# Kernel optimization log

Hardware: AMD Instinct MI355X
Metric: run time of the kernel (lower is better)

## Reference

```python
import jax, jax.numpy as jnp
import numpy as np

D_MODEL = 1024
NHEAD = 16
DK = D_MODEL // NHEAD  # 64
B, S = 2, 2048


def setup_inputs() -> dict:
    key = jax.random.key(0)
    ks = jax.random.split(key, 8)
    Q = jax.random.normal(ks[0], (B, S, D_MODEL), dtype=jnp.float32)
    K = jax.random.normal(ks[1], (B, S, D_MODEL), dtype=jnp.float32)
    V = jax.random.normal(ks[2], (B, S, D_MODEL), dtype=jnp.float32)
    additive_mask = jax.random.normal(ks[3], (S, S), dtype=jnp.float32)
    key_padding_mask = jnp.zeros((B, S), dtype=jnp.int32)  # ignored by the module
    # Per-head projection weights, stacked over heads: [H, d_model, dk]
    scale = 1.0 / np.sqrt(D_MODEL)
    WQ = jax.random.normal(ks[4], (NHEAD, D_MODEL, DK), dtype=jnp.float32) * scale
    WK = jax.random.normal(ks[5], (NHEAD, D_MODEL, DK), dtype=jnp.float32) * scale
    WV = jax.random.normal(ks[6], (NHEAD, D_MODEL, DK), dtype=jnp.float32) * scale
    WO = jax.random.normal(ks[7], (D_MODEL, D_MODEL), dtype=jnp.float32) * scale
    return {"Q": Q, "K": K, "V": V, "additive_mask": additive_mask,
            "key_padding_mask": key_padding_mask,
            "WQ": WQ, "WK": WK, "WV": WV, "WO": WO}


def reference(Q, K, V, additive_mask, key_padding_mask, WQ, WK, WV, WO):
    # Per-head projections, batched over heads: [B, H, S, dk]
    q = jnp.einsum('bsd,hdk->bhsk', Q, WQ)
    k = jnp.einsum('bsd,hdk->bhsk', K, WK)
    v = jnp.einsum('bsd,hdk->bhsk', V, WV)
    # scores: [B, H, S, S]; mask broadcasts over batch and head
    scores = jnp.einsum('bhqk,bhsk->bhqs', q, k) / np.sqrt(DK)
    scores = scores + additive_mask[None, None, :, :]
    attn = jax.nn.softmax(scores, axis=-1)
    o = jnp.einsum('bhqs,bhsk->bhqk', attn, v)  # [B, H, S, dk]
    # concat heads in head order == transpose + reshape to [B, S, H*dk]
    o = o.transpose(0, 2, 1, 3).reshape(Q.shape[0], Q.shape[1], D_MODEL)
    return o @ WO
```

## Files before the change

kernel.cpp:

```cpp
#include <hip/hip_runtime.h>
#include <hip/hip_bf16.h>
#include <stdint.h>

#define D_MODEL 1024
#define NHEAD 16
#define DKH 64
#define BATCH 2
#define SEQ 2048
#define LOG2E 1.44269504088896f

typedef __bf16 bf16_t;
typedef __bf16 bf16x8 __attribute__((ext_vector_type(8)));
typedef float f32x4 __attribute__((ext_vector_type(4)));

__device__ __forceinline__ float fast_exp2(float x) {
#if __has_builtin(__builtin_amdgcn_exp2f)
  return __builtin_amdgcn_exp2f(x);
#else
  return exp2f(x);
#endif
}

__device__ __forceinline__ void gload_lds16(const bf16_t* g, bf16_t* l) {
  auto gp = (const __attribute__((address_space(1))) void*)(uintptr_t)g;
  auto lp = (__attribute__((address_space(3))) void*)(uintptr_t)l;
  __builtin_amdgcn_global_load_lds(gp, lp, 16, 0, 0);
}

__global__ void k_cvtw(const float* __restrict__ WQ, const float* __restrict__ WK,
                       const float* __restrict__ WV, const float* __restrict__ WO,
                       bf16_t* __restrict__ wt) {
  int j = blockIdx.x * 256 + threadIdx.x;
  int d = j & 1023, n = j >> 10;
  if (n < 3072) {
    int proj = n >> 10, h = (n >> 6) & 15, k = n & 63;
    const float* w = proj == 0 ? WQ : (proj == 1 ? WK : WV);
    float scale = proj == 0 ? (0.125f * LOG2E) : 1.0f;
    wt[j] = (bf16_t)(w[(h << 16) + (d << 6) + k] * scale);
  } else {
    wt[j] = (bf16_t)WO[(d << 10) + (n - 3072)];
  }
}

__global__ void k_maskg(const float* __restrict__ M, bf16_t* __restrict__ Mf) {
  int t = blockIdx.x * 256 + threadIdx.x;
  int c = t & 3, lane = (t >> 2) & 63;
  int kvt = (t >> 8) & 31, qt16 = t >> 13;
  int q = qt16 * 16 + (lane & 15);
  int kv = kvt * 64 + c * 16 + ((lane >> 4) << 2);
  float4 m4 = *reinterpret_cast<const float4*>(M + (size_t)q * SEQ + kv);
  bf16_t o[4];
  o[0] = (bf16_t)(m4.x * LOG2E); o[1] = (bf16_t)(m4.y * LOG2E);
  o[2] = (bf16_t)(m4.z * LOG2E); o[3] = (bf16_t)(m4.w * LOG2E);
  *reinterpret_cast<ushort4*>(Mf + (size_t)t * 4) = *reinterpret_cast<ushort4*>(o);
}

__device__ __forceinline__ int vperm(int u) {
  return ((u >> 5) << 5) | (((u >> 2) & 3) << 3) | (((u >> 4) & 1) << 2) | (u & 3);
}

__global__ __launch_bounds__(256)
void k_gemm_qkv(const float* __restrict__ Qs, const float* __restrict__ Ks32,
                const float* __restrict__ Vs32, const bf16_t* __restrict__ Bt,
                bf16_t* __restrict__ qh, bf16_t* __restrict__ Kf,
                bf16_t* __restrict__ Vf) {
  __shared__ __align__(16) bf16_t As[128 * 32];
  __shared__ __align__(16) bf16_t Bs[128 * 32];
  const int tid = threadIdx.x;
  const int lane = tid & 63, wave = tid >> 6;
  const int g = lane >> 4, lr = lane & 15;
  const int bid = blockIdx.x;
  const int xcd = bid & 7, jj = bid >> 3;
  const int bm = xcd * 4 + (jj & 3);
  const int bn = jj >> 2;
  const int pn = bn >> 3;
  const float* Ap32 = pn == 0 ? Qs : (pn == 1 ? Ks32 : Vs32);
  const int wm = (wave >> 1) << 6, wn = (wave & 1) << 6;
  const int arow = tid >> 1, ako = (tid & 1) << 4;
  const float* aptr = Ap32 + (size_t)(bm * 128 + arow) * 1024 + ako;
  f32x4 acc[4][4] = {};

  float4 fA0 = *reinterpret_cast<const float4*>(aptr);
  float4 fA1 = *reinterpret_cast<const float4*>(aptr + 4);
  float4 fA2 = *reinterpret_cast<const float4*>(aptr + 8);
  float4 fA3 = *reinterpret_cast<const float4*>(aptr + 12);

  for (int kt = 0; kt < 1024; kt += 32) {
#pragma unroll
    for (int cc = 0; cc < 2; cc++) {
      int c = tid + cc * 256;
      int row = c >> 2, ko = (c & 3) << 3;
      gload_lds16(Bt + (size_t)(bn * 128 + row) * 1024 + kt + ko, Bs + c * 8);
    }
    {
      bf16x8 o0, o1;
      o0[0] = (bf16_t)fA0.x; o0[1] = (bf16_t)fA0.y; o0[2] = (bf16_t)fA0.z; o0[3] = (bf16_t)fA0.w;
      o0[4] = (bf16_t)fA1.x; o0[5] = (bf16_t)fA1.y; o0[6] = (bf16_t)fA1.z; o0[7] = (bf16_t)fA1.w;
      o1[0] = (bf16_t)fA2.x; o1[1] = (bf16_t)fA2.y; o1[2] = (bf16_t)fA2.z; o1[3] = (bf16_t)fA2.w;
      o1[4] = (bf16_t)fA3.x; o1[5] = (bf16_t)fA3.y; o1[6] = (bf16_t)fA3.z; o1[7] = (bf16_t)fA3.w;
      *reinterpret_cast<bf16x8*>(As + arow * 32 + ako) = o0;
      *reinterpret_cast<bf16x8*>(As + arow * 32 + ako + 8) = o1;
    }
    if (kt + 32 < 1024) {
      const float* np = aptr + kt + 32;
      fA0 = *reinterpret_cast<const float4*>(np);
      fA1 = *reinterpret_cast<const float4*>(np + 4);
      fA2 = *reinterpret_cast<const float4*>(np + 8);
      fA3 = *reinterpret_cast<const float4*>(np + 12);
    }
    __syncthreads();
    bf16x8 af[4], bfr[4];
#pragma unroll
    for (int t = 0; t < 4; t++)
      af[t] = *reinterpret_cast<const bf16x8*>(As + (wm + t * 16 + lr) * 32 + g * 8);
#pragma unroll
    for (int t = 0; t < 4; t++)
      bfr[t] = *reinterpret_cast<const bf16x8*>(Bs + (wn + t * 16 + lr) * 32 + g * 8);
    __builtin_amdgcn_s_setprio(1);
#pragma unroll
    for (int i = 0; i < 4; i++)
#pragma unroll
      for (int j = 0; j < 4; j++)
        acc[i][j] = __builtin_amdgcn_mfma_f32_16x16x32_bf16(af[i], bfr[j], acc[i][j], 0, 0, 0);
    __builtin_amdgcn_s_setprio(0);
    __syncthreads();
  }

#pragma unroll
  for (int i = 0; i < 4; i++)
#pragma unroll
    for (int j = 0; j < 4; j++)
#pragma unroll
      for (int e = 0; e < 4; e++) {
        int row = (bm << 7) + wm + i * 16 + g * 4 + e;
        int col = ((bn & 7) << 7) + wn + j * 16 + lr;
        float v = acc[i][j][e];
        int b = row >> 11, s = row & 2047, h = col >> 6, d = col & 63;
        size_t tilebase = ((size_t)(((b << 4) + h) * 32) + (s >> 6)) * 4096;
        if (pn == 0) {
          qh[((size_t)(((b << 4) + h) * SEQ + s) << 6) + d] = (bf16_t)v;
        } else if (pn == 1) {
          int r = s & 63, u = (d >> 3) ^ (r & 7), e2 = d & 7;
          Kf[tilebase + r * 64 + u * 8 + e2] = (bf16_t)v;
        } else {
          int c6 = vperm(s & 63);
          int u = (c6 >> 3) ^ (d & 7), e2 = c6 & 7;
          Vf[tilebase + d * 64 + u * 8 + e2] = (bf16_t)v;
        }
      }
}

__global__ __launch_bounds__(256)
void k_gemm_wo(const bf16_t* __restrict__ A, const bf16_t* __restrict__ Bt,
               float* __restrict__ C) {
  __shared__ __align__(16) bf16_t As[64 * 32];
  __shared__ __align__(16) bf16_t Bs[128 * 32];
  const int tid = threadIdx.x;
  const int lane = tid & 63, wave = tid >> 6;
  const int g = lane >> 4, lr = lane & 15;
  const int bid = blockIdx.x;
  const int xcd = bid & 7, jj = bid >> 3;
  const int bm = xcd * 8 + (jj & 7);
  const int bn = jj >> 3;
  const int wm = (wave >> 1) << 5, wn = (wave & 1) << 6;
  f32x4 acc[2][4] = {};

  for (int kt = 0; kt < 1024; kt += 32) {
    {
      int row = tid >> 2, ko = (tid & 3) << 3;
      gload_lds16(A + (size_t)(bm * 64 + row) * 1024 + kt + ko, As + tid * 8);
    }
#pragma unroll
    for (int cc = 0; cc < 2; cc++) {
      int c = tid + cc * 256;
      int row = c >> 2, ko = (c & 3) << 3;
      gload_lds16(Bt + (size_t)(bn * 128 + row) * 1024 + kt + ko, Bs + c * 8);
    }
    __syncthreads();
    bf16x8 af[2], bfr[4];
#pragma unroll
    for (int t = 0; t < 2; t++)
      af[t] = *reinterpret_cast<const bf16x8*>(As + (wm + t * 16 + lr) * 32 + g * 8);
#pragma unroll
    for (int t = 0; t < 4; t++)
      bfr[t] = *reinterpret_cast<const bf16x8*>(Bs + (wn + t * 16 + lr) * 32 + g * 8);
    __builtin_amdgcn_s_setprio(1);
#pragma unroll
    for (int i = 0; i < 2; i++)
#pragma unroll
      for (int j = 0; j < 4; j++)
        acc[i][j] = __builtin_amdgcn_mfma_f32_16x16x32_bf16(af[i], bfr[j], acc[i][j], 0, 0, 0);
    __builtin_amdgcn_s_setprio(0);
    __syncthreads();
  }
#pragma unroll
  for (int i = 0; i < 2; i++)
#pragma unroll
    for (int j = 0; j < 4; j++)
#pragma unroll
      for (int e = 0; e < 4; e++) {
        int row = (bm << 6) + wm + i * 16 + g * 4 + e;
        int col = (bn << 7) + wn + j * 16 + lr;
        C[(size_t)row * D_MODEL + col] = acc[i][j][e];
      }
}

__global__ __launch_bounds__(512)
void k_attn4(const bf16_t* __restrict__ Qh, const bf16_t* __restrict__ Kf,
             const bf16_t* __restrict__ Vf, const bf16_t* __restrict__ Mf,
             bf16_t* __restrict__ O) {
  __shared__ __align__(16) bf16_t Ks[2][64 * 64];
  __shared__ __align__(16) bf16_t Vs[2][64 * 64];
  const int bid = blockIdx.x;
  const int xcd = bid & 7, loc = bid >> 3;
  const int bh = xcd * 4 + (loc >> 4);
  const int qtile = loc & 15;
  const int b = bh >> 4, h = bh & 15;
  const int tid = threadIdx.x, wave = tid >> 6, lane = tid & 63;
  const int g = lane >> 4, lr = lane & 15;
  const int qbase = qtile * 128 + wave * 16;
  const bf16_t* qp = Qh + (size_t)bh * SEQ * DKH;
  const bf16_t* kfp = Kf + (size_t)bh * 32 * 4096;
  const bf16_t* vfp = Vf + (size_t)bh * 32 * 4096;
  const int qt16 = qtile * 8 + wave;
  const bf16_t* mp = Mf + ((size_t)qt16 * 32 * 64 + lane) * 16;

  bf16x8 aq[2];
#pragma unroll
  for (int ks = 0; ks < 2; ks++)
    aq[ks] = *reinterpret_cast<const bf16x8*>(
        qp + (size_t)(qbase + lr) * DKH + ks * 32 + g * 8);

  f32x4 oacc[4] = {};
  f32x4 lacc = {};
  const bf16_t onev = (bf16_t)1.0f;
  const bf16x8 ones = {onev, onev, onev, onev, onev, onev, onev, onev};

  auto stage = [&](int buf, int kt) {
    gload_lds16(kfp + (size_t)kt * 4096 + tid * 8, &Ks[buf][tid * 8]);
    gload_lds16(vfp + (size_t)kt * 4096 + tid * 8, &Vs[buf][tid * 8]);
  };

  stage(0, 0);
  bf16x8 mva = *reinterpret_cast<const bf16x8*>(mp);
  bf16x8 mvb = *reinterpret_cast<const bf16x8*>(mp + 8);
  __syncthreads();

  for (int it = 0; it < SEQ / 64; ++it) {
    const int cur = it & 1;
    if (it + 1 < SEQ / 64) stage(cur ^ 1, it + 1);
    bf16x8 mna = mva, mnb = mvb;
    if (it + 1 < SEQ / 64) {
      const bf16_t* mn = mp + (size_t)(it + 1) * 1024;
      mna = *reinterpret_cast<const bf16x8*>(mn);
      mnb = *reinterpret_cast<const bf16x8*>(mn + 8);
    }

    const bf16_t* kb = Ks[cur];
    const bf16_t* vb = Vs[cur];

    f32x4 p[4];
#pragma unroll
    for (int c = 0; c < 4; c++) {
      int r = c * 16 + lr;
      bf16x8 bk0 = *reinterpret_cast<const bf16x8*>(kb + r * 64 + ((g ^ (lr & 7)) << 3));
      bf16x8 bk1 = *reinterpret_cast<const bf16x8*>(kb + r * 64 + (((4 + g) ^ (lr & 7)) << 3));
      __builtin_amdgcn_s_setprio(1);
      f32x4 a = {};
      a = __builtin_amdgcn_mfma_f32_16x16x32_bf16(bk0, aq[0], a, 0, 0, 0);
      a = __builtin_amdgcn_mfma_f32_16x16x32_bf16(bk1, aq[1], a, 0, 0, 0);
      __builtin_amdgcn_s_setprio(0);
      p[c] = a;
    }

    bf16x8 pa[2];
#pragma unroll
    for (int c = 0; c < 4; c++)
#pragma unroll
      for (int e = 0; e < 4; e++) {
        int idx = c * 4 + e;
        float mk = (float)(idx < 8 ? mva[idx] : mvb[idx - 8]);
        float x = p[c][e] + mk;
        float pe = fast_exp2(fminf(x, 60.f));
        pa[c >> 1][(c & 1) * 4 + e] = (bf16_t)pe;
      }

    lacc = __builtin_amdgcn_mfma_f32_16x16x32_bf16(pa[0], ones, lacc, 0, 0, 0);
    lacc = __builtin_amdgcn_mfma_f32_16x16x32_bf16(pa[1], ones, lacc, 0, 0, 0);

#pragma unroll
    for (int c2 = 0; c2 < 4; c2++) {
      int r = c2 * 16 + lr;
      bf16x8 bv0 = *reinterpret_cast<const bf16x8*>(vb + r * 64 + ((g ^ (lr & 7)) << 3));
      bf16x8 bv1 = *reinterpret_cast<const bf16x8*>(vb + r * 64 + (((4 + g) ^ (lr & 7)) << 3));
      __builtin_amdgcn_s_setprio(1);
      oacc[c2] = __builtin_amdgcn_mfma_f32_16x16x32_bf16(pa[0], bv0, oacc[c2], 0, 0, 0);
      oacc[c2] = __builtin_amdgcn_mfma_f32_16x16x32_bf16(pa[1], bv1, oacc[c2], 0, 0, 0);
      __builtin_amdgcn_s_setprio(0);
    }
    __syncthreads();
    mva = mna; mvb = mnb;
  }

  float inv[4];
#pragma unroll
  for (int e = 0; e < 4; e++) inv[e] = 1.0f / lacc[e];
#pragma unroll
  for (int c2 = 0; c2 < 4; c2++)
#pragma unroll
    for (int e = 0; e < 4; e++) {
      float v = oacc[c2][e] * inv[e];
      int row = qbase + g * 4 + e;
      int col = (h << 6) + c2 * 16 + lr;
      O[(size_t)(b * SEQ + row) * D_MODEL + col] = (bf16_t)v;
    }
}

extern "C" void kernel_launch(void* const* d_in, const int* in_sizes, int n_in,
                              void* d_out, int out_size, void* d_ws, size_t ws_size,
                              hipStream_t stream) {
  const float* Q  = (const float*)d_in[0];
  const float* K  = (const float*)d_in[1];
  const float* V  = (const float*)d_in[2];
  const float* M  = (const float*)d_in[3];
  const float* WQ = (const float*)d_in[5];
  const float* WK = (const float*)d_in[6];
  const float* WV = (const float*)d_in[7];
  const float* WO = (const float*)d_in[8];

  char* ws = (char*)d_ws;
  const size_t MB = 1 << 20;
  bf16_t* Mf    = (bf16_t*)(ws + 24 * MB);
  bf16_t* WqkvT = (bf16_t*)(ws + 32 * MB);
  bf16_t* WoT   = (bf16_t*)(ws + 38 * MB);
  bf16_t* qh    = (bf16_t*)(ws + 40 * MB);
  bf16_t* Kf    = (bf16_t*)(ws + 48 * MB);
  bf16_t* Vf    = (bf16_t*)(ws + 56 * MB);
  bf16_t* Ob    = (bf16_t*)(ws + 64 * MB);

  k_maskg<<<4096, 256, 0, stream>>>(M, Mf);
  k_cvtw<<<16384, 256, 0, stream>>>(WQ, WK, WV, WO, WqkvT);

  k_gemm_qkv<<<768, 256, 0, stream>>>(Q, K, V, WqkvT, qh, Kf, Vf);

  k_attn4<<<512, 512, 0, stream>>>(qh, Kf, Vf, Mf, Ob);

  k_gemm_wo<<<512, 256, 0, stream>>>(Ob, WoT, (float*)d_out);
}
```

Measured before the change: 145.8 us.

## Pre-tile weights into k-chunk-major blocks for contiguous loads and conflict-free LDS reads

The weight conversion kernel now writes the bf16 weights pre-tiled as [n-block][k-tile][8-element group][row][8], so each 128x32 B tile is one contiguous 8 KB chunk. Both GEMMs load it with fully contiguous global_load_lds and read fragments from an LDS layout of [group][row][8]. The QKV GEMM's A tile is stored in the same group-major layout. The aim is to make global reads fully coalesced and remove LDS bank conflicts from the 64-byte row stride, at the cost of more complex indexing in the weight conversion.

```diff
diff --git a/kernel.cpp b/kernel.cpp
--- a/kernel.cpp
+++ b/kernel.cpp
@@ -31,14 +31,22 @@
                        const float* __restrict__ WV, const float* __restrict__ WO,
                        bf16_t* __restrict__ wt) {
   int j = blockIdx.x * 256 + threadIdx.x;
-  int d = j & 1023, n = j >> 10;
-  if (n < 3072) {
+  if (j < 3072 * 1024) {
+    int bn = j >> 17, kt = (j >> 12) & 31, u = (j >> 10) & 3;
+    int row = (j >> 3) & 127, e = j & 7;
+    int n = bn * 128 + row;
+    int d = kt * 32 + u * 8 + e;
     int proj = n >> 10, h = (n >> 6) & 15, k = n & 63;
     const float* w = proj == 0 ? WQ : (proj == 1 ? WK : WV);
     float scale = proj == 0 ? (0.125f * LOG2E) : 1.0f;
     wt[j] = (bf16_t)(w[(h << 16) + (d << 6) + k] * scale);
   } else {
-    wt[j] = (bf16_t)WO[(d << 10) + (n - 3072)];
+    int j2 = j - 3072 * 1024;
+    int bn = j2 >> 17, kt = (j2 >> 12) & 31, u = (j2 >> 10) & 3;
+    int row = (j2 >> 3) & 127, e = j2 & 7;
+    int n = bn * 128 + row;
+    int d = kt * 32 + u * 8 + e;
+    wt[j] = (bf16_t)WO[(d << 10) + n];
   }
 }
 
@@ -64,8 +72,8 @@
                 const float* __restrict__ Vs32, const bf16_t* __restrict__ Bt,
                 bf16_t* __restrict__ qh, bf16_t* __restrict__ Kf,
                 bf16_t* __restrict__ Vf) {
-  __shared__ __align__(16) bf16_t As[128 * 32];
-  __shared__ __align__(16) bf16_t Bs[128 * 32];
+  __shared__ __align__(16) bf16_t As[4 * 128 * 8];
+  __shared__ __align__(16) bf16_t Bs[4 * 128 * 8];
   const int tid = threadIdx.x;
   const int lane = tid & 63, wave = tid >> 6;
   const int g = lane >> 4, lr = lane & 15;
@@ -75,8 +83,9 @@
   const int bn = jj >> 2;
   const int pn = bn >> 3;
   const float* Ap32 = pn == 0 ? Qs : (pn == 1 ? Ks32 : Vs32);
+  const bf16_t* btile = Bt + (size_t)bn * 32 * 4096;
   const int wm = (wave >> 1) << 6, wn = (wave & 1) << 6;
-  const int arow = tid >> 1, ako = (tid & 1) << 4;
+  const int arow = tid >> 1, au0 = (tid & 1) << 1, ako = (tid & 1) << 4;
   const float* aptr = Ap32 + (size_t)(bm * 128 + arow) * 1024 + ako;
   f32x4 acc[4][4] = {};
 
@@ -86,11 +95,11 @@
   float4 fA3 = *reinterpret_cast<const float4*>(aptr + 12);
 
   for (int kt = 0; kt < 1024; kt += 32) {
+    const int ktt = kt >> 5;
 #pragma unroll
     for (int cc = 0; cc < 2; cc++) {
       int c = tid + cc * 256;
-      int row = c >> 2, ko = (c & 3) << 3;
-      gload_lds16(Bt + (size_t)(bn * 128 + row) * 1024 + kt + ko, Bs + c * 8);
+      gload_lds16(btile + (size_t)ktt * 4096 + c * 8, Bs + c * 8);
     }
     {
       bf16x8 o0, o1;
@@ -98,8 +107,8 @@
       o0[4] = (bf16_t)fA1.x; o0[5] = (bf16_t)fA1.y; o0[6] = (bf16_t)fA1.z; o0[7] = (bf16_t)fA1.w;
       o1[0] = (bf16_t)fA2.x; o1[1] = (bf16_t)fA2.y; o1[2] = (bf16_t)fA2.z; o1[3] = (bf16_t)fA2.w;
       o1[4] = (bf16_t)fA3.x; o1[5] = (bf16_t)fA3.y; o1[6] = (bf16_t)fA3.z; o1[7] = (bf16_t)fA3.w;
-      *reinterpret_cast<bf16x8*>(As + arow * 32 + ako) = o0;
-      *reinterpret_cast<bf16x8*>(As + arow * 32 + ako + 8) = o1;
+      *reinterpret_cast<bf16x8*>(As + (au0 * 128 + arow) * 8) = o0;
+      *reinterpret_cast<bf16x8*>(As + ((au0 + 1) * 128 + arow) * 8) = o1;
     }
     if (kt + 32 < 1024) {
       const float* np = aptr + kt + 32;
@@ -112,10 +121,10 @@
     bf16x8 af[4], bfr[4];
 #pragma unroll
     for (int t = 0; t < 4; t++)
-      af[t] = *reinterpret_cast<const bf16x8*>(As + (wm + t * 16 + lr) * 32 + g * 8);
+      af[t] = *reinterpret_cast<const bf16x8*>(As + (g * 128 + wm + t * 16 + lr) * 8);
 #pragma unroll
     for (int t = 0; t < 4; t++)
-      bfr[t] = *reinterpret_cast<const bf16x8*>(Bs + (wn + t * 16 + lr) * 32 + g * 8);
+      bfr[t] = *reinterpret_cast<const bf16x8*>(Bs + (g * 128 + wn + t * 16 + lr) * 8);
     __builtin_amdgcn_s_setprio(1);
 #pragma unroll
     for (int i = 0; i < 4; i++)
@@ -154,7 +163,7 @@
 void k_gemm_wo(const bf16_t* __restrict__ A, const bf16_t* __restrict__ Bt,
                float* __restrict__ C) {
   __shared__ __align__(16) bf16_t As[64 * 32];
-  __shared__ __align__(16) bf16_t Bs[128 * 32];
+  __shared__ __align__(16) bf16_t Bs[4 * 128 * 8];
   const int tid = threadIdx.x;
   const int lane = tid & 63, wave = tid >> 6;
   const int g = lane >> 4, lr = lane & 15;
@@ -162,10 +171,12 @@
   const int xcd = bid & 7, jj = bid >> 3;
   const int bm = xcd * 8 + (jj & 7);
   const int bn = jj >> 3;
+  const bf16_t* btile = Bt + (size_t)bn * 32 * 4096;
   const int wm = (wave >> 1) << 5, wn = (wave & 1) << 6;
   f32x4 acc[2][4] = {};
 
   for (int kt = 0; kt < 1024; kt += 32) {
+    const int ktt = kt >> 5;
     {
       int row = tid >> 2, ko = (tid & 3) << 3;
       gload_lds16(A + (size_t)(bm * 64 + row) * 1024 + kt + ko, As + tid * 8);
@@ -173,8 +184,7 @@
 #pragma unroll
     for (int cc = 0; cc < 2; cc++) {
       int c = tid + cc * 256;
-      int row = c >> 2, ko = (c & 3) << 3;
-      gload_lds16(Bt + (size_t)(bn * 128 + row) * 1024 + kt + ko, Bs + c * 8);
+      gload_lds16(btile + (size_t)ktt * 4096 + c * 8, Bs + c * 8);
     }
     __syncthreads();
     bf16x8 af[2], bfr[4];
@@ -183,7 +193,7 @@
       af[t] = *reinterpret_cast<const bf16x8*>(As + (wm + t * 16 + lr) * 32 + g * 8);
 #pragma unroll
     for (int t = 0; t < 4; t++)
-      bfr[t] = *reinterpret_cast<const bf16x8*>(Bs + (wn + t * 16 + lr) * 32 + g * 8);
+      bfr[t] = *reinterpret_cast<const bf16x8*>(Bs + (g * 128 + wn + t * 16 + lr) * 8);
     __builtin_amdgcn_s_setprio(1);
 #pragma unroll
     for (int i = 0; i < 2; i++)
```

Measured after the change: 135.7 us. -6.9%, faster.
